# Kernel optimization log

Measured on AMD Instinct MI355X. Metric: run time of the kernel, lower is better.

## Reference

```python
import jax, jax.numpy as jnp
import numpy as np

N = 100000       # nodes
E = 1600000      # edges (avg degree 16)
W_IN = 256
W_HID = 64
T = 4            # node types
K = 10           # diffusion hops (num_layers)
ALPHA = 0.1
EPS = 1e-12


def setup_inputs() -> dict:
    key = jax.random.key(0)
    k1, k2, k3, k4, k5 = jax.random.split(key, 5)
    X = jax.random.normal(k1, (N, W_IN), dtype=jnp.float32)
    W_enc = jax.random.normal(k2, (W_IN, W_HID), dtype=jnp.float32) * 0.1  # xavier-ish scale
    b_enc = jnp.zeros((W_HID,), dtype=jnp.float32)
    gaussian_sample = jax.random.normal(k3, (N * W_HID,), dtype=jnp.float32)
    edge_index = jax.random.randint(k4, (2, E), 0, N, dtype=jnp.int64)
    node_type = jax.random.randint(k5, (N,), 0, T, dtype=jnp.int64)
    return {"X": X, "W_enc": W_enc, "b_enc": b_enc,
            "gaussian_sample": gaussian_sample,
            "edge_index": edge_index, "node_type": node_type}


def _l2_normalize_rows(x):
    # F.normalize(x, p=2, dim=1)
    n = jnp.sqrt(jnp.sum(x * x, axis=1, keepdims=True))
    return x / jnp.maximum(n, EPS)


def reference(X, W_enc, b_enc, gaussian_sample, edge_index, node_type):
    # --- type-aware encoding: Linear + L2 row-normalize (act='l2') ---
    H = X @ W_enc + b_enc                       # [N, W_HID]
    H = _l2_normalize_rows(H)

    # --- per-type statistics (vectorized segment reduce over node types) ---
    counts = jax.ops.segment_sum(jnp.ones((N,), H.dtype), node_type, num_segments=T)  # [T]
    mean_t = jax.ops.segment_sum(H, node_type, num_segments=T) / counts[:, None]      # [T, W_HID]
    dev2 = (H - mean_t[node_type]) ** 2
    # original: 1/sqrt(n_i - 1) * sum((H_i - mean_i)^2)  (sum, not mean — faithful)
    std_t = jax.ops.segment_sum(dev2, node_type, num_segments=T) / jnp.sqrt(counts - 1.0)[:, None]

    tilde_H = (H - mean_t[node_type]) / std_t[node_type]  # [N, W_HID]

    # --- wasserstein loss: W1 between flattened embeddings and a standard gaussian
    # sample of equal size (scipy wasserstein_distance == mean |sorted diffs|).
    # Original detaches embeddings (numpy), so stop_gradient the whole loss.
    emb = jax.lax.stop_gradient(tilde_H).reshape(-1)
    loss = jax.lax.stop_gradient(
        jnp.mean(jnp.abs(jnp.sort(gaussian_sample) - jnp.sort(emb))))

    # dropout with training=False -> identity

    # --- PPR diffusion: K steps of row-normalized SpMM with restart ---
    src, dst = edge_index[0], edge_index[1]
    deg = jax.ops.segment_sum(jnp.ones((E,), H.dtype), dst, num_segments=N)
    deg = jnp.maximum(deg, 1.0)                 # avoid div-by-zero for isolated nodes
    edge_norm = (1.0 / deg)[dst]                # D^{-1} A (row normalization)

    Z = tilde_H
    for _ in range(K):
        agg = jax.ops.segment_sum(Z[src] * edge_norm[:, None], dst, num_segments=N)
        Z = (1.0 - ALPHA) * agg + ALPHA * tilde_H

    # --- de-normalize back with per-type stats, then L2 row-normalize ---
    Z = Z * std_t[node_type] + mean_t[node_type]
    Z = _l2_normalize_rows(Z)
    return (Z, loss)
```

## Files before the change

kernel.cpp:

```cpp
#include <hip/hip_runtime.h>
#include <math.h>

#define WH 64
#define WIN 256
#define TT 4
#define ALPHA_C 0.1f
#define STATS_GRID 256
#define BN 64
#define KC 32
#define XS_STRIDE (KC + 4)
#define BINS 16384
#define BIN_SCALE 1024.0f
#define HG 256
#define SB 128
#define ST 256

typedef unsigned short ushortT;

__device__ __forceinline__ unsigned pack_bf16(float a, float b) {
  unsigned ua = __float_as_uint(a), ub = __float_as_uint(b);
  ua = (ua + 0x7FFFu + ((ua >> 16) & 1u)) >> 16;
  ub = ((ub + 0x7FFFu + ((ub >> 16) & 1u)) >> 16) << 16;
  return (ua & 0xFFFFu) | ub;
}
__device__ __forceinline__ float bf_lo(unsigned p) { return __uint_as_float(p << 16); }
__device__ __forceinline__ float bf_hi(unsigned p) { return __uint_as_float(p & 0xFFFF0000u); }

__global__ __launch_bounds__(256) void k_encode(const float* __restrict__ X,
                                                const float* __restrict__ W,
                                                const float* __restrict__ bias,
                                                float* __restrict__ H, int N) {
  __shared__ __align__(16) float Xs[BN * XS_STRIDE];
  __shared__ __align__(16) float Ws[KC * WH];
  int tid = threadIdx.x;
  int tn = tid >> 4, tc = tid & 15;
  int nodeBase = blockIdx.x * BN;
  float acc[4][4] = {};
  for (int k0 = 0; k0 < WIN; k0 += KC) {
    __syncthreads();
    const float4* Wg4 = (const float4*)(W + (size_t)k0 * WH);
    float4* Ws4 = (float4*)Ws;
    Ws4[tid] = Wg4[tid];
    Ws4[tid + 256] = Wg4[tid + 256];
#pragma unroll
    for (int i = 0; i < 2; ++i) {
      int idx = tid + i * 256;
      int ln = idx >> 3, f4 = idx & 7;
      int node = nodeBase + ln;
      if (node < N) {
        *(float4*)&Xs[ln * XS_STRIDE + f4 * 4] =
            *(const float4*)(X + (size_t)node * WIN + k0 + f4 * 4);
      }
    }
    __syncthreads();
    for (int kk = 0; kk < KC; kk += 4) {
      float4 b0 = *(const float4*)&Ws[(kk + 0) * WH + tc * 4];
      float4 b1 = *(const float4*)&Ws[(kk + 1) * WH + tc * 4];
      float4 b2 = *(const float4*)&Ws[(kk + 2) * WH + tc * 4];
      float4 b3 = *(const float4*)&Ws[(kk + 3) * WH + tc * 4];
#pragma unroll
      for (int i = 0; i < 4; ++i) {
        float4 a = *(const float4*)&Xs[(tn * 4 + i) * XS_STRIDE + kk];
        acc[i][0] += a.x * b0.x + a.y * b1.x + a.z * b2.x + a.w * b3.x;
        acc[i][1] += a.x * b0.y + a.y * b1.y + a.z * b2.y + a.w * b3.y;
        acc[i][2] += a.x * b0.z + a.y * b1.z + a.z * b2.z + a.w * b3.z;
        acc[i][3] += a.x * b0.w + a.y * b1.w + a.z * b2.w + a.w * b3.w;
      }
    }
  }
  float4 bv = *(const float4*)(bias + tc * 4);
#pragma unroll
  for (int i = 0; i < 4; ++i) {
    float h0 = acc[i][0] + bv.x, h1 = acc[i][1] + bv.y;
    float h2 = acc[i][2] + bv.z, h3 = acc[i][3] + bv.w;
    float s = h0 * h0 + h1 * h1 + h2 * h2 + h3 * h3;
    s += __shfl_xor(s, 1, 64);
    s += __shfl_xor(s, 2, 64);
    s += __shfl_xor(s, 4, 64);
    s += __shfl_xor(s, 8, 64);
    float r = 1.0f / fmaxf(sqrtf(s), 1e-12f);
    int node = nodeBase + tn * 4 + i;
    if (node < N) {
      float4 o = {h0 * r, h1 * r, h2 * r, h3 * r};
      *(float4*)(H + (size_t)node * WH + tc * 4) = o;
    }
  }
}

__global__ __launch_bounds__(256) void k_stats(const float* __restrict__ H,
                                               const int* __restrict__ nt,
                                               float* __restrict__ psum,
                                               float* __restrict__ psq,
                                               float* __restrict__ pcnt, int NW) {
  __shared__ float ls[TT * WH], ls2[TT * WH];
  __shared__ float lc[TT];
  ls[threadIdx.x] = 0.0f;
  ls2[threadIdx.x] = 0.0f;
  if (threadIdx.x < TT) lc[threadIdx.x] = 0.0f;
  __syncthreads();
  for (int i = blockIdx.x * 256 + threadIdx.x; i < NW; i += STATS_GRID * 256) {
    int nn = i >> 6, d = i & 63;
    int t = nt[nn];
    float v = H[i];
    atomicAdd(&ls[t * WH + d], v);
    atomicAdd(&ls2[t * WH + d], v * v);
    if (d == 0) atomicAdd(&lc[t], 1.0f);
  }
  __syncthreads();
  psum[blockIdx.x * 256 + threadIdx.x] = ls[threadIdx.x];
  psq[blockIdx.x * 256 + threadIdx.x] = ls2[threadIdx.x];
  if (threadIdx.x < TT) pcnt[blockIdx.x * TT + threadIdx.x] = lc[threadIdx.x];
}

__global__ __launch_bounds__(256) void k_reduce_stats(const float* __restrict__ psum,
                                                      const float* __restrict__ psq,
                                                      const float* __restrict__ pcnt,
                                                      float* __restrict__ mean,
                                                      float* __restrict__ stdv,
                                                      float* __restrict__ counts) {
  __shared__ float c[TT];
  if (threadIdx.x < TT) {
    float s = 0.0f;
    for (int b = 0; b < STATS_GRID; ++b) s += pcnt[b * TT + threadIdx.x];
    counts[threadIdx.x] = s;
    c[threadIdx.x] = s;
  }
  __syncthreads();
  float s = 0.0f, q = 0.0f;
  for (int b = 0; b < STATS_GRID; ++b) {
    s += psum[b * 256 + threadIdx.x];
    q += psq[b * 256 + threadIdx.x];
  }
  float n = c[threadIdx.x >> 6];
  float m = s / n;
  mean[threadIdx.x] = m;
  stdv[threadIdx.x] = (q - s * s / n) / sqrtf(n - 1.0f);
}

__global__ __launch_bounds__(256) void k_tilde_hist(float* __restrict__ H,
                                                    const int* __restrict__ nt,
                                                    const float* __restrict__ mean,
                                                    const float* __restrict__ stdv,
                                                    ushortT* __restrict__ tb,
                                                    unsigned* __restrict__ pe, int NW) {
  __shared__ unsigned hist[BINS];
  for (int b = threadIdx.x; b < BINS; b += 256) hist[b] = 0;
  __syncthreads();
  for (int i = blockIdx.x * 256 + threadIdx.x; i < NW; i += HG * 256) {
    int nn = i >> 6, d = i & 63;
    int t = nt[nn];
    float v = (H[i] - mean[t * WH + d]) / stdv[t * WH + d];
    H[i] = v;
    unsigned u = __float_as_uint(v);
    tb[i] = (ushortT)((u + 0x7FFFu + ((u >> 16) & 1u)) >> 16);
    int b = (int)((v + 8.0f) * BIN_SCALE);
    b = min(max(b, 0), BINS - 1);
    atomicAdd(&hist[b], 1u);
  }
  __syncthreads();
  for (int b = threadIdx.x; b < BINS; b += 256)
    pe[(size_t)blockIdx.x * BINS + b] = hist[b];
}

__global__ __launch_bounds__(256) void k_histG(const float* __restrict__ g,
                                               unsigned* __restrict__ pg, int M) {
  __shared__ unsigned hist[BINS];
  for (int b = threadIdx.x; b < BINS; b += 256) hist[b] = 0;
  __syncthreads();
  for (int i = blockIdx.x * 256 + threadIdx.x; i < M; i += HG * 256) {
    float v = g[i];
    int b = (int)((v + 8.0f) * BIN_SCALE);
    b = min(max(b, 0), BINS - 1);
    atomicAdd(&hist[b], 1u);
  }
  __syncthreads();
  for (int b = threadIdx.x; b < BINS; b += 256)
    pg[(size_t)blockIdx.x * BINS + b] = hist[b];
}

__global__ __launch_bounds__(256) void k_diff(const unsigned* __restrict__ pg,
                                              const unsigned* __restrict__ pe,
                                              int* __restrict__ diff) {
  int b = blockIdx.x * 256 + threadIdx.x;
  int s = 0;
  for (int p = 0; p < HG; ++p)
    s += (int)pg[(size_t)p * BINS + b] - (int)pe[(size_t)p * BINS + b];
  diff[b] = s;
}

__global__ __launch_bounds__(1024) void k_wass(const int* __restrict__ diff,
                                               float* __restrict__ out, int M, int NW) {
  int tid = threadIdx.x;
  int lo = tid * (BINS / 1024);
  int d[BINS / 1024];
  int s = 0;
#pragma unroll
  for (int i = 0; i < BINS / 1024; ++i) {
    d[i] = diff[lo + i];
    s += d[i];
  }
  __shared__ int sc[1024];
  sc[tid] = s;
  __syncthreads();
  for (int st = 1; st < 1024; st <<= 1) {
    int v = (tid >= st) ? sc[tid - st] : 0;
    __syncthreads();
    sc[tid] += v;
    __syncthreads();
  }
  int run = sc[tid] - s;
  long long a = 0;
#pragma unroll
  for (int i = 0; i < BINS / 1024; ++i) {
    run += d[i];
    a += (long long)(run < 0 ? -run : run);
  }
  __shared__ long long rd[1024];
  rd[tid] = a;
  __syncthreads();
  for (int st = 512; st > 0; st >>= 1) {
    if (tid < st) rd[tid] += rd[tid + st];
    __syncthreads();
  }
  if (tid == 0) out[NW] = (float)((double)rd[0] * (1.0 / (double)BIN_SCALE) / (double)M);
}

__global__ __launch_bounds__(256) void k_degi(const int* __restrict__ dst,
                                              unsigned* __restrict__ degi, int E) {
  int e = blockIdx.x * 256 + threadIdx.x;
  if (e < E) atomicAdd(&degi[dst[e]], 1u);
}

__global__ __launch_bounds__(ST) void k_scan_part(const unsigned* __restrict__ in,
                                                  unsigned* __restrict__ bsum, int L) {
  int C = (L + SB * ST - 1) / (SB * ST);
  int base = (blockIdx.x * ST + threadIdx.x) * C;
  int hi = min(base + C, L);
  unsigned s = 0;
  for (int i = base; i < hi; ++i) s += in[i];
  __shared__ unsigned red[ST];
  red[threadIdx.x] = s;
  __syncthreads();
  for (int st = ST / 2; st > 0; st >>= 1) {
    if (threadIdx.x < st) red[threadIdx.x] += red[threadIdx.x + st];
    __syncthreads();
  }
  if (threadIdx.x == 0) bsum[blockIdx.x] = red[0];
}
__global__ __launch_bounds__(ST) void k_scan_mid(unsigned* __restrict__ bsum) {
  __shared__ unsigned ts[ST];
  unsigned v = (threadIdx.x < SB) ? bsum[threadIdx.x] : 0u;
  ts[threadIdx.x] = v;
  __syncthreads();
  for (int st = 1; st < ST; st <<= 1) {
    unsigned u = (threadIdx.x >= (unsigned)st) ? ts[threadIdx.x - st] : 0u;
    __syncthreads();
    ts[threadIdx.x] += u;
    __syncthreads();
  }
  if (threadIdx.x < SB) bsum[threadIdx.x] = ts[threadIdx.x] - v;
}
__global__ __launch_bounds__(ST) void k_scan_apply(const unsigned* __restrict__ in,
                                                   const unsigned* __restrict__ bsum,
                                                   unsigned* __restrict__ outp, int L) {
  int C = (L + SB * ST - 1) / (SB * ST);
  int base = (blockIdx.x * ST + threadIdx.x) * C;
  int hi = min(base + C, L);
  unsigned s = 0;
  for (int i = base; i < hi; ++i) s += in[i];
  __shared__ unsigned ts[ST];
  ts[threadIdx.x] = s;
  __syncthreads();
  for (int st = 1; st < ST; st <<= 1) {
    unsigned u = (threadIdx.x >= (unsigned)st) ? ts[threadIdx.x - st] : 0u;
    __syncthreads();
    ts[threadIdx.x] += u;
    __syncthreads();
  }
  unsigned run = bsum[blockIdx.x] + ts[threadIdx.x] - s;
  for (int i = base; i < hi; ++i) {
    unsigned c = in[i];
    outp[i] = run;
    run += c;
  }
}

__global__ __launch_bounds__(256) void k_build(const int* __restrict__ src,
                                               const int* __restrict__ dst,
                                               const unsigned* __restrict__ off,
                                               unsigned* __restrict__ cur,
                                               unsigned* __restrict__ esrc, int E) {
  int e = blockIdx.x * 256 + threadIdx.x;
  if (e >= E) return;
  int t = dst[e];
  unsigned p = off[t] + atomicAdd(&cur[t], 1u);
  esrc[p] = (unsigned)src[e];
}

__global__ __launch_bounds__(256) void k_spmm(const unsigned* __restrict__ off,
                                              const unsigned* __restrict__ degi,
                                              const unsigned* __restrict__ esrc,
                                              const ushortT* __restrict__ Zb,
                                              const float* __restrict__ tilde,
                                              ushortT* __restrict__ Zn, int N) {
  int wv = threadIdx.x >> 6, lane = threadIdx.x & 63;
  int n = blockIdx.x * 4 + wv;
  if (n >= N) return;
  int g = lane >> 3, c = lane & 7;
  unsigned st = off[n], dg = degi[n];
  float a[8] = {};
  for (unsigned e = g; e < dg; e += 8) {
    unsigned s = esrc[st + e];
    uint4 v = *((const uint4*)(Zb + (size_t)s * WH) + c);
    a[0] += bf_lo(v.x); a[1] += bf_hi(v.x);
    a[2] += bf_lo(v.y); a[3] += bf_hi(v.y);
    a[4] += bf_lo(v.z); a[5] += bf_hi(v.z);
    a[6] += bf_lo(v.w); a[7] += bf_hi(v.w);
  }
#pragma unroll
  for (int m = 8; m <= 32; m <<= 1) {
#pragma unroll
    for (int j = 0; j < 8; ++j) a[j] += __shfl_xor(a[j], m, 64);
  }
  if (g == 0) {
    float wn = (1.0f - ALPHA_C) / fmaxf((float)dg, 1.0f);
    const float4* Tr = (const float4*)(tilde + (size_t)n * WH);
    float4 t0 = Tr[2 * c], t1 = Tr[2 * c + 1];
    float o0 = wn * a[0] + ALPHA_C * t0.x, o1 = wn * a[1] + ALPHA_C * t0.y;
    float o2 = wn * a[2] + ALPHA_C * t0.z, o3 = wn * a[3] + ALPHA_C * t0.w;
    float o4 = wn * a[4] + ALPHA_C * t1.x, o5 = wn * a[5] + ALPHA_C * t1.y;
    float o6 = wn * a[6] + ALPHA_C * t1.z, o7 = wn * a[7] + ALPHA_C * t1.w;
    uint4 p;
    p.x = pack_bf16(o0, o1);
    p.y = pack_bf16(o2, o3);
    p.z = pack_bf16(o4, o5);
    p.w = pack_bf16(o6, o7);
    *((uint4*)(Zn + (size_t)n * WH) + c) = p;
  }
}

__global__ __launch_bounds__(256) void k_final(const ushortT* __restrict__ Zb,
                                               const int* __restrict__ nt,
                                               const float* __restrict__ mean,
                                               const float* __restrict__ stdv,
                                               float* __restrict__ out, int N) {
  int wv = threadIdx.x >> 6, lane = threadIdx.x & 63;
  int n = blockIdx.x * 4 + wv;
  if (n >= N) return;
  int t = nt[n];
  float zv = __uint_as_float((unsigned)Zb[(size_t)n * WH + lane] << 16);
  float z = zv * stdv[t * WH + lane] + mean[t * WH + lane];
  float s = z * z;
#pragma unroll
  for (int off = 32; off > 0; off >>= 1) s += __shfl_xor(s, off, 64);
  float r = 1.0f / fmaxf(sqrtf(s), 1e-12f);
  out[(size_t)n * WH + lane] = z * r;
}

extern "C" void kernel_launch(void* const* d_in, const int* in_sizes, int n_in,
                              void* d_out, int out_size, void* d_ws, size_t ws_size,
                              hipStream_t stream) {
  const float* X = (const float*)d_in[0];
  const float* W = (const float*)d_in[1];
  const float* bias = (const float*)d_in[2];
  const float* g = (const float*)d_in[3];
  const int* ei = (const int*)d_in[4];
  const int* nt = (const int*)d_in[5];

  const int N = in_sizes[5];
  const int E = in_sizes[4] / 2;
  const int M = in_sizes[3];
  const int NW = N * WH;
  const int* srcp = ei;
  const int* dstp = ei + E;

  char* w = (char*)d_ws;
  size_t o = 0;
  auto alloc = [&](size_t bytes) {
    size_t r = o;
    o += (bytes + 255) & ~(size_t)255;
    return r;
  };
  size_t off_stats = alloc(4096);
  size_t off_psum  = alloc((size_t)STATS_GRID * 256 * 4);
  size_t off_psq   = alloc((size_t)STATS_GRID * 256 * 4);
  size_t off_pcnt  = alloc((size_t)STATS_GRID * TT * 4);
  size_t off_diff  = alloc((size_t)BINS * 4);
  size_t off_bsum  = alloc((size_t)SB * 4);
  size_t off_degi  = alloc((size_t)N * 4);
  size_t off_cur   = alloc((size_t)N * 4);
  size_t off_off   = alloc((size_t)N * 4);
  size_t off_esrc  = alloc((size_t)E * 4);
  size_t off_tilde = alloc((size_t)NW * 4);
  size_t off_tbf   = alloc((size_t)NW * 2);
  size_t off_bufA  = alloc((size_t)NW * 4);
  size_t off_bufB  = alloc((size_t)NW * 4);

  float* counts = (float*)(w + off_stats + 0);
  float* mean   = (float*)(w + off_stats + 256);
  float* stdv   = (float*)(w + off_stats + 1280);
  float* psum   = (float*)(w + off_psum);
  float* psq    = (float*)(w + off_psq);
  float* pcnt   = (float*)(w + off_pcnt);
  int* diff     = (int*)(w + off_diff);
  unsigned* bsum = (unsigned*)(w + off_bsum);
  unsigned* degi = (unsigned*)(w + off_degi);
  unsigned* cur  = (unsigned*)(w + off_cur);
  unsigned* offp = (unsigned*)(w + off_off);
  unsigned* esrc = (unsigned*)(w + off_esrc);
  float* tilde   = (float*)(w + off_tilde);
  ushortT* tbf   = (ushortT*)(w + off_tbf);
  unsigned* pg   = (unsigned*)(w + off_bufA);
  unsigned* pe   = (unsigned*)(w + off_bufB);
  ushortT* ZA    = (ushortT*)(w + off_bufA);
  ushortT* ZB    = (ushortT*)(w + off_bufB);
  float* out = (float*)d_out;

  hipMemsetAsync(w + off_degi, 0, off_cur - off_degi + (size_t)N * 4, stream);

  k_encode<<<(N + BN - 1) / BN, 256, 0, stream>>>(X, W, bias, tilde, N);

  k_stats<<<STATS_GRID, 256, 0, stream>>>(tilde, nt, psum, psq, pcnt, NW);
  k_reduce_stats<<<1, 256, 0, stream>>>(psum, psq, pcnt, mean, stdv, counts);

  k_tilde_hist<<<HG, 256, 0, stream>>>(tilde, nt, mean, stdv, tbf, pe, NW);
  k_histG<<<HG, 256, 0, stream>>>(g, pg, M);

  k_diff<<<BINS / 256, 256, 0, stream>>>(pg, pe, diff);
  k_wass<<<1, 1024, 0, stream>>>(diff, out, M, NW);

  k_degi<<<(E + 255) / 256, 256, 0, stream>>>(dstp, degi, E);
  k_scan_part<<<SB, ST, 0, stream>>>(degi, bsum, N);
  k_scan_mid<<<1, ST, 0, stream>>>(bsum);
  k_scan_apply<<<SB, ST, 0, stream>>>(degi, bsum, offp, N);
  k_build<<<(E + 255) / 256, 256, 0, stream>>>(srcp, dstp, offp, cur, esrc, E);

  const ushortT* Zc = tbf;
  for (int k = 0; k < 10; ++k) {
    ushortT* Zn = (k & 1) ? ZB : ZA;
    k_spmm<<<(N + 3) / 4, 256, 0, stream>>>(offp, degi, esrc, Zc, tilde, Zn, N);
    Zc = Zn;
  }

  k_final<<<(N + 3) / 4, 256, 0, stream>>>(Zc, nt, mean, stdv, out, N);
}
```

Baseline: 1.099 ms.

## Retile encoder GEMM to 8x8 register tiles with transposed X in LDS

The encoder GEMM now gives each thread an 8x8 output tile, with 128 threads covering 128 nodes per block instead of 4x4 tiles over 64 nodes. X is staged through registers and stored transposed in shared memory so every k-step reads contiguous float4 fragments of A and B. This raises arithmetic intensity per shared-memory load. In exchange it uses more registers per thread (64 accumulators), launches fewer blocks, and the transposed stores may cause LDS bank conflicts.

Result: no change. 1.085 ms (-1.3%).

```diff
diff --git a/kernel.cpp b/kernel.cpp
--- a/kernel.cpp
+++ b/kernel.cpp
@@ -6,9 +6,10 @@
 #define TT 4
 #define ALPHA_C 0.1f
 #define STATS_GRID 256
-#define BN 64
 #define KC 32
-#define XS_STRIDE (KC + 4)
+#define ENC_T 128
+#define ENC_BN 128
+#define XT_STRIDE 132
 #define BINS 16384
 #define BIN_SCALE 1024.0f
 #define HG 256
@@ -26,63 +27,80 @@
 __device__ __forceinline__ float bf_lo(unsigned p) { return __uint_as_float(p << 16); }
 __device__ __forceinline__ float bf_hi(unsigned p) { return __uint_as_float(p & 0xFFFF0000u); }
 
-__global__ __launch_bounds__(256) void k_encode(const float* __restrict__ X,
-                                                const float* __restrict__ W,
-                                                const float* __restrict__ bias,
-                                                float* __restrict__ H, int N) {
-  __shared__ __align__(16) float Xs[BN * XS_STRIDE];
+__global__ __launch_bounds__(128, 4) void k_encode(const float* __restrict__ X,
+                                                   const float* __restrict__ W,
+                                                   const float* __restrict__ bias,
+                                                   float* __restrict__ H, int N) {
+  __shared__ __align__(16) float XsT[KC * XT_STRIDE];
   __shared__ __align__(16) float Ws[KC * WH];
   int tid = threadIdx.x;
-  int tn = tid >> 4, tc = tid & 15;
-  int nodeBase = blockIdx.x * BN;
-  float acc[4][4] = {};
+  int ng = tid >> 3, cg = tid & 7;
+  int nodeBase = blockIdx.x * ENC_BN;
+  float acc[8][8] = {};
   for (int k0 = 0; k0 < WIN; k0 += KC) {
     __syncthreads();
     const float4* Wg4 = (const float4*)(W + (size_t)k0 * WH);
     float4* Ws4 = (float4*)Ws;
-    Ws4[tid] = Wg4[tid];
-    Ws4[tid + 256] = Wg4[tid + 256];
-#pragma unroll
-    for (int i = 0; i < 2; ++i) {
-      int idx = tid + i * 256;
+#pragma unroll
+    for (int j = 0; j < 4; ++j) Ws4[tid + j * 128] = Wg4[tid + j * 128];
+    float4 xv[8];
+#pragma unroll
+    for (int i = 0; i < 8; ++i) {
+      int idx = tid + i * 128;
       int ln = idx >> 3, f4 = idx & 7;
       int node = nodeBase + ln;
-      if (node < N) {
-        *(float4*)&Xs[ln * XS_STRIDE + f4 * 4] =
-            *(const float4*)(X + (size_t)node * WIN + k0 + f4 * 4);
-      }
+      if (node < N)
+        xv[i] = *(const float4*)(X + (size_t)node * WIN + k0 + f4 * 4);
+      else
+        xv[i] = make_float4(0.f, 0.f, 0.f, 0.f);
     }
-    __syncthreads();
-    for (int kk = 0; kk < KC; kk += 4) {
-      float4 b0 = *(const float4*)&Ws[(kk + 0) * WH + tc * 4];
-      float4 b1 = *(const float4*)&Ws[(kk + 1) * WH + tc * 4];
-      float4 b2 = *(const float4*)&Ws[(kk + 2) * WH + tc * 4];
-      float4 b3 = *(const float4*)&Ws[(kk + 3) * WH + tc * 4];
-#pragma unroll
-      for (int i = 0; i < 4; ++i) {
-        float4 a = *(const float4*)&Xs[(tn * 4 + i) * XS_STRIDE + kk];
-        acc[i][0] += a.x * b0.x + a.y * b1.x + a.z * b2.x + a.w * b3.x;
-        acc[i][1] += a.x * b0.y + a.y * b1.y + a.z * b2.y + a.w * b3.y;
-        acc[i][2] += a.x * b0.z + a.y * b1.z + a.z * b2.z + a.w * b3.z;
-        acc[i][3] += a.x * b0.w + a.y * b1.w + a.z * b2.w + a.w * b3.w;
-      }
+#pragma unroll
+    for (int i = 0; i < 8; ++i) {
+      int idx = tid + i * 128;
+      int ln = idx >> 3, f4 = idx & 7;
+      float* p = &XsT[(f4 * 4) * XT_STRIDE + ln];
+      p[0] = xv[i].x;
+      p[XT_STRIDE] = xv[i].y;
+      p[2 * XT_STRIDE] = xv[i].z;
+      p[3 * XT_STRIDE] = xv[i].w;
     }
-  }
-  float4 bv = *(const float4*)(bias + tc * 4);
-#pragma unroll
-  for (int i = 0; i < 4; ++i) {
-    float h0 = acc[i][0] + bv.x, h1 = acc[i][1] + bv.y;
-    float h2 = acc[i][2] + bv.z, h3 = acc[i][3] + bv.w;
-    float s = h0 * h0 + h1 * h1 + h2 * h2 + h3 * h3;
+    __syncthreads();
+#pragma unroll 4
+    for (int k = 0; k < KC; ++k) {
+      float4 a0 = *(const float4*)&XsT[k * XT_STRIDE + ng * 8];
+      float4 a1 = *(const float4*)&XsT[k * XT_STRIDE + ng * 8 + 4];
+      float4 b0 = *(const float4*)&Ws[k * WH + cg * 8];
+      float4 b1 = *(const float4*)&Ws[k * WH + cg * 8 + 4];
+      float av[8] = {a0.x, a0.y, a0.z, a0.w, a1.x, a1.y, a1.z, a1.w};
+      float bb[8] = {b0.x, b0.y, b0.z, b0.w, b1.x, b1.y, b1.z, b1.w};
+#pragma unroll
+      for (int i = 0; i < 8; ++i)
+#pragma unroll
+        for (int j = 0; j < 8; ++j) acc[i][j] += av[i] * bb[j];
+    }
+  }
+  float4 bb0 = *(const float4*)(bias + cg * 8);
+  float4 bb1 = *(const float4*)(bias + cg * 8 + 4);
+  float bv[8] = {bb0.x, bb0.y, bb0.z, bb0.w, bb1.x, bb1.y, bb1.z, bb1.w};
+#pragma unroll
+  for (int i = 0; i < 8; ++i) {
+    float h[8];
+    float s = 0.f;
+#pragma unroll
+    for (int j = 0; j < 8; ++j) {
+      h[j] = acc[i][j] + bv[j];
+      s += h[j] * h[j];
+    }
     s += __shfl_xor(s, 1, 64);
     s += __shfl_xor(s, 2, 64);
     s += __shfl_xor(s, 4, 64);
-    s += __shfl_xor(s, 8, 64);
     float r = 1.0f / fmaxf(sqrtf(s), 1e-12f);
-    int node = nodeBase + tn * 4 + i;
+    int node = nodeBase + ng * 8 + i;
     if (node < N) {
-      float4 o = {h0 * r, h1 * r, h2 * r, h3 * r};
-      *(float4*)(H + (size_t)node * WH + tc * 4) = o;
+      float4 o0 = {h[0] * r, h[1] * r, h[2] * r, h[3] * r};
+      float4 o1 = {h[4] * r, h[5] * r, h[6] * r, h[7] * r};
+      *(float4*)(H + (size_t)node * WH + cg * 8) = o0;
+      *(float4*)(H + (size_t)node * WH + cg * 8 + 4) = o1;
     }
   }
 }
@@ -418,7 +436,7 @@
 
   hipMemsetAsync(w + off_degi, 0, off_cur - off_degi + (size_t)N * 4, stream);
 
-  k_encode<<<(N + BN - 1) / BN, 256, 0, stream>>>(X, W, bias, tilde, N);
+  k_encode<<<(N + ENC_BN - 1) / ENC_BN, ENC_T, 0, stream>>>(X, W, bias, tilde, N);
 
   k_stats<<<STATS_GRID, 256, 0, stream>>>(tilde, nt, psum, psq, pcnt, NW);
   k_reduce_stats<<<1, 256, 0, stream>>>(psum, psq, pcnt, mean, stdv, counts);
```
